# Optimization experiments

Measured on AMD Instinct MI355X. Metric: run time of the kernel, lower is better.

Reference implementation:

```python
import jax, jax.numpy as jnp
import numpy as np

N_NODES = 4096
IN_FEAT = 256
N_HEADS = 8
N_HIDDEN = 64  # out_features // n_heads
NEG_SLOPE = 0.2
EDGE_PROB = 0.05


def setup_inputs() -> dict:
    key = jax.random.key(0)
    k1, k2, k3, k4 = jax.random.split(key, 4)
    h = jax.random.normal(k1, (N_NODES, IN_FEAT), dtype=jnp.float32)
    # binary adjacency mask [N, N, 1] (broadcast over heads), as in the torch asserts
    adj_mat = (jax.random.uniform(k2, (N_NODES, N_NODES, 1)) < EDGE_PROB).astype(jnp.float32)
    # nn.Linear(in_features, n_heads*n_hidden, bias=False) weight: [H*F, in]
    W = jax.random.normal(k3, (N_HEADS * N_HIDDEN, IN_FEAT), dtype=jnp.float32) / np.sqrt(IN_FEAT)
    # nn.Linear(2*n_hidden, 1, bias=False) weight, flattened: [2*F]
    a = jax.random.normal(k4, (2 * N_HIDDEN,), dtype=jnp.float32) / np.sqrt(2 * N_HIDDEN)
    return {"h": h, "adj_mat": adj_mat, "W": W, "a": a}


def reference(h, adj_mat, W, a):
    n = h.shape[0]
    # g: [N, H, F]
    g = (h @ W.T).reshape(n, N_HEADS, N_HIDDEN)
    # attn(cat[g_i, g_j]) == a_l . g_i + a_r . g_j  (linear, no bias)
    a_l = a[:N_HIDDEN]
    a_r = a[N_HIDDEN:]
    el = jnp.einsum('ihf,f->ih', g, a_l)  # [N, H]
    er = jnp.einsum('jhf,f->jh', g, a_r)  # [N, H]
    e = jax.nn.leaky_relu(el[:, None, :] + er[None, :, :], NEG_SLOPE)  # [N, N, H]
    # note: original multiplies scores by adjacency (not masked_fill)
    e = e * adj_mat  # adj broadcasts over heads
    att = jax.nn.softmax(e, axis=1)  # softmax over source nodes j
    # dropout is identity at eval (dropout_rate=0.0)
    out = jnp.einsum('ijh,jhf->ihf', att, g)  # [N, H, F]
    return out.reshape(n, N_HEADS * N_HIDDEN)
```

## Files before the change

### kernel.cpp

```cpp
#include <hip/hip_runtime.h>

#define N_NODES 4096
#define IN_FEAT 256
#define N_HEADS 8
#define N_HIDDEN 64
#define OUT_FEAT (N_HEADS * N_HIDDEN)
#define NEG_SLOPE 0.2f

typedef _Float16 half8 __attribute__((ext_vector_type(8)));
typedef float floatx4 __attribute__((ext_vector_type(4)));

__global__ __launch_bounds__(256) void produce(
    const float* __restrict__ H, const float* __restrict__ adj,
    const float* __restrict__ Wt, const float* __restrict__ a,
    _Float16* __restrict__ GT16, float* __restrict__ elT,
    float* __restrict__ eR1, float* __restrict__ eR2,
    unsigned long long* __restrict__ bits) {
  __shared__ _Float16 SM[4 * 64 * 64];
  const int t = threadIdx.x;
  const int bx = blockIdx.x, by = blockIdx.y;

  if (by >= 8) {
    const int c = bx * 8 + (by - 8);
    const size_t W0 = (size_t)c * 512;
    const int wv = t >> 6, lane = t & 63;
    for (int k0 = 0; k0 < 128; k0 += 8) {
      float v[8];
#pragma unroll
      for (int k = 0; k < 8; ++k)
        v[k] = adj[(W0 + wv * 128 + k0 + k) * 64 + lane];
#pragma unroll
      for (int k = 0; k < 8; ++k) {
        unsigned long long m = __ballot(v[k] != 0.f);
        if (lane == 0) bits[W0 + wv * 128 + k0 + k] = m;
      }
    }
    return;
  }

  _Float16* Ah = SM;
  _Float16* Al = SM + 4096;
  _Float16* Bh = SM + 8192;
  _Float16* Bl = SM + 12288;
  const int w = t >> 6, l = t & 63;
  const int n16 = l & 15, q = l >> 4;
  const int bi = bx, bo = by;
  const int m0 = bi * 64 + w * 16;

  floatx4 acc[4];
#pragma unroll
  for (int ct = 0; ct < 4; ++ct) acc[ct] = (floatx4)0.f;

  for (int kc = 0; kc < 4; ++kc) {
    if (kc) __syncthreads();
#pragma unroll
    for (int p = 0; p < 4; ++p) {
      const int idx = p * 256 + t;
      const int r = idx >> 4;
      const int c4 = (idx & 15) << 2;
      const int dst = r * 64 + ((((idx & 15) >> 1)) ^ (r & 7)) * 8 + (idx & 1) * 4;
      float4 hv = *(const float4*)(H + (size_t)(bi * 64 + r) * IN_FEAT + kc * 64 + c4);
      float4 wv = *(const float4*)(Wt + (size_t)(bo * 64 + r) * IN_FEAT + kc * 64 + c4);
      union { _Float16 h[4]; int2 d; } hh_, hl_, wh_, wl_;
      hh_.h[0] = (_Float16)hv.x; hh_.h[1] = (_Float16)hv.y;
      hh_.h[2] = (_Float16)hv.z; hh_.h[3] = (_Float16)hv.w;
      hl_.h[0] = (_Float16)(hv.x - (float)hh_.h[0]);
      hl_.h[1] = (_Float16)(hv.y - (float)hh_.h[1]);
      hl_.h[2] = (_Float16)(hv.z - (float)hh_.h[2]);
      hl_.h[3] = (_Float16)(hv.w - (float)hh_.h[3]);
      wh_.h[0] = (_Float16)wv.x; wh_.h[1] = (_Float16)wv.y;
      wh_.h[2] = (_Float16)wv.z; wh_.h[3] = (_Float16)wv.w;
      wl_.h[0] = (_Float16)(wv.x - (float)wh_.h[0]);
      wl_.h[1] = (_Float16)(wv.y - (float)wh_.h[1]);
      wl_.h[2] = (_Float16)(wv.z - (float)wh_.h[2]);
      wl_.h[3] = (_Float16)(wv.w - (float)wh_.h[3]);
      *(int2*)&Ah[dst] = hh_.d;
      *(int2*)&Al[dst] = hl_.d;
      *(int2*)&Bh[dst] = wh_.d;
      *(int2*)&Bl[dst] = wl_.d;
    }
    __syncthreads();
#pragma unroll
    for (int ks = 0; ks < 2; ++ks) {
      const int ao = (w * 16 + n16) * 64 + (((ks << 2) + q) ^ (n16 & 7)) * 8;
      half8 Afh = *(const half8*)&Ah[ao];
      half8 Afl = *(const half8*)&Al[ao];
#pragma unroll
      for (int ct = 0; ct < 4; ++ct) {
        const int bofs = (ct * 16 + n16) * 64 + (((ks << 2) + q) ^ (n16 & 7)) * 8;
        half8 Bfh = *(const half8*)&Bh[bofs];
        half8 Bfl = *(const half8*)&Bl[bofs];
        acc[ct] = __builtin_amdgcn_mfma_f32_16x16x32_f16(Afh, Bfh, acc[ct], 0, 0, 0);
        acc[ct] = __builtin_amdgcn_mfma_f32_16x16x32_f16(Afl, Bfh, acc[ct], 0, 0, 0);
        acc[ct] = __builtin_amdgcn_mfma_f32_16x16x32_f16(Afh, Bfl, acc[ct], 0, 0, 0);
      }
    }
  }

  float aLv[4], aRv[4];
#pragma unroll
  for (int ct = 0; ct < 4; ++ct) {
    aLv[ct] = a[ct * 16 + n16];
    aRv[ct] = a[64 + ct * 16 + n16];
  }
#pragma unroll
  for (int reg = 0; reg < 4; ++reg) {
    float sl = 0.f, sr = 0.f;
#pragma unroll
    for (int ct = 0; ct < 4; ++ct) {
      sl = fmaf(acc[ct][reg], aLv[ct], sl);
      sr = fmaf(acc[ct][reg], aRv[ct], sr);
    }
#pragma unroll
    for (int off = 1; off < 16; off <<= 1) {
      sl += __shfl_xor(sl, off);
      sr += __shfl_xor(sr, off);
    }
    if (n16 == 0) {
      const int rowi = m0 + q * 4 + reg;
      elT[(size_t)bo * N_NODES + rowi] = sl;
      eR1[(size_t)bo * N_NODES + rowi] = __expf(sr);
      eR2[(size_t)bo * N_NODES + rowi] = __expf(0.2f * sr);
    }
  }

  __syncthreads();
  _Float16* LG = SM;
#pragma unroll
  for (int ct = 0; ct < 4; ++ct)
#pragma unroll
    for (int reg = 0; reg < 4; ++reg)
      LG[(w * 16 + q * 4 + reg) * 72 + ct * 16 + n16] = (_Float16)acc[ct][reg];
  __syncthreads();
  {
    const int f = t >> 2, jq = t & 3;
    union { _Float16 hh[16]; int4 v[2]; } u;
#pragma unroll
    for (int k = 0; k < 16; ++k) u.hh[k] = LG[(jq * 16 + k) * 72 + f];
    _Float16* dst = GT16 + (size_t)(bo * 64 + f) * N_NODES + bi * 64 + jq * 16;
    *(int4*)dst = u.v[0];
    *(int4*)(dst + 8) = u.v[1];
  }
}

__global__ __launch_bounds__(512) void attn_v5(
    const unsigned long long* __restrict__ bits, const _Float16* __restrict__ GT16,
    const float* __restrict__ elT, const float* __restrict__ eR1,
    const float* __restrict__ eR2, float* __restrict__ out) {
  __shared__ __align__(16) unsigned char GtRaw[2][2][8192];
  __shared__ float eRs1[2][2][64], eRs2[2][2][64];
  __shared__ unsigned long long bitsS[2][2][64];
  __shared__ float eL1s[64], eL2s[64];
  __shared__ float ZBuf[2][64];

  const int t = threadIdx.x;
  const int ib = blockIdx.x, h = blockIdx.y;
  const int i0 = ib * 64;
  const int w = t >> 6, l = t & 63, n16 = l & 15, q = l >> 4;
  const int jh = w >> 2, rt = w & 3;

  auto stage = [&](int par, int step) {
    const int sf = t >> 3, sseg = t & 7;
#pragma unroll
    for (int g = 0; g < 2; ++g) {
      const _Float16* src =
          GT16 + (size_t)(h * 64 + sf) * N_NODES + g * 2048 + step * 64 + sseg * 8;
      int4 v = *(const int4*)src;
      *(int4*)&((_Float16*)GtRaw[g][par])[sf * 64 + (sseg ^ (sf & 7)) * 8] = v;
    }
    if (t < 128) {
      eRs1[t >> 6][par][t & 63] =
          eR1[(size_t)h * N_NODES + (t >> 6) * 2048 + step * 64 + (t & 63)];
    } else if (t < 256) {
      const int u = t - 128;
      eRs2[u >> 6][par][u & 63] =
          eR2[(size_t)h * N_NODES + (u >> 6) * 2048 + step * 64 + (u & 63)];
    } else if (t < 384) {
      const int u = t - 256;
      bitsS[u >> 6][par][u & 63] =
          bits[(size_t)(i0 + (u & 63)) * 64 + (u >> 6) * 32 + step];
    }
  };

  if (t < 64) {
    float e = elT[(size_t)h * N_NODES + i0 + t];
    eL1s[t] = __expf(e);
    eL2s[t] = __expf(0.2f * e);
  }
  stage(0, 0);
  __syncthreads();

  const float eL1 = eL1s[rt * 16 + n16];
  const float eL2 = eL2s[rt * 16 + n16];
  half8 Bones;
#pragma unroll
  for (int k = 0; k < 8; ++k) Bones[k] = (n16 == 0) ? (_Float16)1.f : (_Float16)0.f;

  floatx4 acc[4];
#pragma unroll
  for (int ft = 0; ft < 4; ++ft) acc[ft] = (floatx4)0.f;
  floatx4 acc5 = (floatx4)0.f;

  int par = 0;
  for (int step = 0; step < 32; ++step) {
    if (step + 1 < 32) stage(par ^ 1, step + 1);
    const unsigned long long bv = bitsS[jh][par][rt * 16 + n16];
    const _Float16* gt = (const _Float16*)GtRaw[jh][par];
#pragma unroll
    for (int ks = 0; ks < 2; ++ks) {
      const int j8 = ks * 32 + q * 8;
      const unsigned byte = (unsigned)(bv >> j8) & 0xffu;
      float4 r1a = *(const float4*)&eRs1[jh][par][j8];
      float4 r1b = *(const float4*)&eRs1[jh][par][j8 + 4];
      float4 r2a = *(const float4*)&eRs2[jh][par][j8];
      float4 r2b = *(const float4*)&eRs2[jh][par][j8 + 4];
      float r1[8] = {r1a.x, r1a.y, r1a.z, r1a.w, r1b.x, r1b.y, r1b.z, r1b.w};
      float r2[8] = {r2a.x, r2a.y, r2a.z, r2a.w, r2b.x, r2b.y, r2b.z, r2b.w};
      half8 Af;
#pragma unroll
      for (int k = 0; k < 8; ++k) {
        const float pv = fmaxf(eL1 * r1[k], eL2 * r2[k]);
        const float p = ((byte >> k) & 1u) ? pv : 1.0f;
        Af[k] = (_Float16)p;
      }
#pragma unroll
      for (int ft = 0; ft < 4; ++ft) {
        half8 Bf = *(const half8*)&gt[(ft * 16 + n16) * 64 + (((ks << 2) + q) ^ (n16 & 7)) * 8];
        acc[ft] = __builtin_amdgcn_mfma_f32_16x16x32_f16(Af, Bf, acc[ft], 0, 0, 0);
      }
      acc5 = __builtin_amdgcn_mfma_f32_16x16x32_f16(Af, Bones, acc5, 0, 0, 0);
    }
    __syncthreads();
    par ^= 1;
  }

  float* comb1 = (float*)GtRaw;
  if (jh == 1) {
#pragma unroll
    for (int ft = 0; ft < 4; ++ft)
#pragma unroll
      for (int reg = 0; reg < 4; ++reg)
        comb1[(rt * 16 + q * 4 + reg) * 68 + ft * 16 + n16] = acc[ft][reg];
    if (n16 == 0) {
#pragma unroll
      for (int reg = 0; reg < 4; ++reg) ZBuf[0][rt * 16 + q * 4 + reg] = acc5[reg];
    }
  }
  __syncthreads();
  if (jh == 0) {
#pragma unroll
    for (int ft = 0; ft < 4; ++ft)
#pragma unroll
      for (int reg = 0; reg < 4; ++reg)
        acc[ft][reg] += comb1[(rt * 16 + q * 4 + reg) * 68 + ft * 16 + n16];
    if (n16 == 0) {
#pragma unroll
      for (int reg = 0; reg < 4; ++reg)
        ZBuf[1][rt * 16 + q * 4 + reg] = acc5[reg] + ZBuf[0][rt * 16 + q * 4 + reg];
    }
  }
  __syncthreads();
  if (jh == 0) {
#pragma unroll
    for (int reg = 0; reg < 4; ++reg) {
      const int row = rt * 16 + q * 4 + reg;
      const float invz = 1.f / ZBuf[1][row];
      float* op = out + (size_t)(i0 + row) * OUT_FEAT + h * 64;
#pragma unroll
      for (int ft = 0; ft < 4; ++ft) op[ft * 16 + n16] = acc[ft][reg] * invz;
    }
  }
}

extern "C" void kernel_launch(void* const* d_in, const int* in_sizes, int n_in,
                              void* d_out, int out_size, void* d_ws, size_t ws_size,
                              hipStream_t stream) {
  const float* h   = (const float*)d_in[0];
  const float* adj = (const float*)d_in[1];
  const float* W   = (const float*)d_in[2];
  const float* a   = (const float*)d_in[3];
  float* out = (float*)d_out;

  char* ws = (char*)d_ws;
  _Float16* GT16 = (_Float16*)ws;
  unsigned long long* bits = (unsigned long long*)(ws + 4u * 1024 * 1024);
  float* elT = (float*)(ws + 6u * 1024 * 1024);
  float* eR1 = (float*)(ws + 6u * 1024 * 1024 + 128 * 1024);
  float* eR2 = (float*)(ws + 6u * 1024 * 1024 + 256 * 1024);

  produce<<<dim3(64, 16), 256, 0, stream>>>(h, adj, W, a, GT16, elT, eR1, eR2, bits);
  attn_v5<<<dim3(64, 8), 512, 0, stream>>>(bits, GT16, elT, eR1, eR2, out);
}
```

Measured before the change: 169.2 us.

## Halve attention block rows, store exp factors in fp16, use packed half math

```diff
diff --git a/kernel.cpp b/kernel.cpp
--- a/kernel.cpp
+++ b/kernel.cpp
@@ -8,13 +8,14 @@
 #define NEG_SLOPE 0.2f
 
 typedef _Float16 half8 __attribute__((ext_vector_type(8)));
+typedef _Float16 h2 __attribute__((ext_vector_type(2)));
 typedef float floatx4 __attribute__((ext_vector_type(4)));
 
 __global__ __launch_bounds__(256) void produce(
     const float* __restrict__ H, const float* __restrict__ adj,
     const float* __restrict__ Wt, const float* __restrict__ a,
     _Float16* __restrict__ GT16, float* __restrict__ elT,
-    float* __restrict__ eR1, float* __restrict__ eR2,
+    _Float16* __restrict__ eR1h, _Float16* __restrict__ eR2h,
     unsigned long long* __restrict__ bits) {
   __shared__ _Float16 SM[4 * 64 * 64];
   const int t = threadIdx.x;
@@ -119,8 +120,8 @@
     if (n16 == 0) {
       const int rowi = m0 + q * 4 + reg;
       elT[(size_t)bo * N_NODES + rowi] = sl;
-      eR1[(size_t)bo * N_NODES + rowi] = __expf(sr);
-      eR2[(size_t)bo * N_NODES + rowi] = __expf(0.2f * sr);
+      eR1h[(size_t)bo * N_NODES + rowi] = (_Float16)__expf(sr);
+      eR2h[(size_t)bo * N_NODES + rowi] = (_Float16)__expf(0.2f * sr);
     }
   }
 
@@ -143,55 +144,53 @@
   }
 }
 
-__global__ __launch_bounds__(512) void attn_v5(
+__global__ __launch_bounds__(256) void attn_v6(
     const unsigned long long* __restrict__ bits, const _Float16* __restrict__ GT16,
-    const float* __restrict__ elT, const float* __restrict__ eR1,
-    const float* __restrict__ eR2, float* __restrict__ out) {
-  __shared__ __align__(16) unsigned char GtRaw[2][2][8192];
-  __shared__ float eRs1[2][2][64], eRs2[2][2][64];
-  __shared__ unsigned long long bitsS[2][2][64];
-  __shared__ float eL1s[64], eL2s[64];
-  __shared__ float ZBuf[2][64];
+    const float* __restrict__ elT, const _Float16* __restrict__ eR1h,
+    const _Float16* __restrict__ eR2h, float* __restrict__ out) {
+  __shared__ __align__(16) _Float16 Gt[2][2][4096];
+  __shared__ __align__(16) _Float16 eRs1[2][2][64];
+  __shared__ __align__(16) _Float16 eRs2[2][2][64];
+  __shared__ uint2 bitsS[2][2][32];
+  __shared__ float eL1s[32], eL2s[32];
+  __shared__ float Zh1[32], Zfull[32];
 
   const int t = threadIdx.x;
   const int ib = blockIdx.x, h = blockIdx.y;
-  const int i0 = ib * 64;
+  const int i0 = ib * 32;
   const int w = t >> 6, l = t & 63, n16 = l & 15, q = l >> 4;
-  const int jh = w >> 2, rt = w & 3;
-
-  auto stage = [&](int par, int step) {
-    const int sf = t >> 3, sseg = t & 7;
-#pragma unroll
-    for (int g = 0; g < 2; ++g) {
-      const _Float16* src =
-          GT16 + (size_t)(h * 64 + sf) * N_NODES + g * 2048 + step * 64 + sseg * 8;
-      int4 v = *(const int4*)src;
-      *(int4*)&((_Float16*)GtRaw[g][par])[sf * 64 + (sseg ^ (sf & 7)) * 8] = v;
-    }
-    if (t < 128) {
-      eRs1[t >> 6][par][t & 63] =
-          eR1[(size_t)h * N_NODES + (t >> 6) * 2048 + step * 64 + (t & 63)];
-    } else if (t < 256) {
-      const int u = t - 128;
-      eRs2[u >> 6][par][u & 63] =
-          eR2[(size_t)h * N_NODES + (u >> 6) * 2048 + step * 64 + (u & 63)];
-    } else if (t < 384) {
-      const int u = t - 256;
-      bitsS[u >> 6][par][u & 63] =
-          bits[(size_t)(i0 + (u & 63)) * 64 + (u >> 6) * 32 + step];
-    }
-  };
-
-  if (t < 64) {
+  const int rt = w & 1, jh = w >> 1;
+
+  const int gjh = t >> 7, sf = (t >> 1) & 63, hrow = t & 1;
+  const _Float16* gsrc = GT16 + (size_t)(h * 64 + sf) * N_NODES + gjh * 2048 + hrow * 32;
+  const int era = (t >> 3) & 1, erjh = t >> 4, erseg = t & 7;
+  const int bro = (t - 32) & 31, brjh = (t - 32) >> 5;
+
+  if (t < 32) {
     float e = elT[(size_t)h * N_NODES + i0 + t];
     eL1s[t] = __expf(e);
     eL2s[t] = __expf(0.2f * e);
   }
-  stage(0, 0);
-  __syncthreads();
-
-  const float eL1 = eL1s[rt * 16 + n16];
-  const float eL2 = eL2s[rt * 16 + n16];
+  {
+#pragma unroll
+    for (int g = 0; g < 4; ++g) {
+      int4 v = *(const int4*)(gsrc + g * 8);
+      *(int4*)&Gt[0][gjh][sf * 64 + ((hrow * 4 + g) ^ (sf & 7)) * 8] = v;
+    }
+    if (t < 32) {
+      const _Float16* esrc = (era ? eR2h : eR1h) + (size_t)h * N_NODES + erjh * 2048 + erseg * 8;
+      int4 v = *(const int4*)esrc;
+      *(int4*)&(era ? eRs2 : eRs1)[0][erjh][erseg * 8] = v;
+    } else if (t < 96) {
+      bitsS[0][brjh][bro] = *(const uint2*)&bits[(size_t)(i0 + bro) * 64 + brjh * 32];
+    }
+  }
+  __syncthreads();
+
+  const _Float16 e1f = (_Float16)eL1s[rt * 16 + n16];
+  const _Float16 e2f = (_Float16)eL2s[rt * 16 + n16];
+  const h2 eL1h2 = {e1f, e1f};
+  const h2 eL2h2 = {e2f, e2f};
   half8 Bones;
 #pragma unroll
   for (int k = 0; k < 8; ++k) Bones[k] = (n16 == 0) ? (_Float16)1.f : (_Float16)0.f;
@@ -203,26 +202,43 @@
 
   int par = 0;
   for (int step = 0; step < 32; ++step) {
-    if (step + 1 < 32) stage(par ^ 1, step + 1);
-    const unsigned long long bv = bitsS[jh][par][rt * 16 + n16];
-    const _Float16* gt = (const _Float16*)GtRaw[jh][par];
+    int4 gv[4]; int4 ev; uint2 bv2;
+    const bool more = (step + 1 < 32);
+    if (more) {
+      const _Float16* gs = gsrc + (size_t)(step + 1) * 64;
+#pragma unroll
+      for (int g = 0; g < 4; ++g) gv[g] = *(const int4*)(gs + g * 8);
+      if (t < 32) {
+        const _Float16* esrc = (era ? eR2h : eR1h) + (size_t)h * N_NODES + erjh * 2048 +
+                               (step + 1) * 64 + erseg * 8;
+        ev = *(const int4*)esrc;
+      } else if (t < 96) {
+        bv2 = *(const uint2*)&bits[(size_t)(i0 + bro) * 64 + brjh * 32 + step + 1];
+      }
+    }
+    const uint2 bw = bitsS[par][jh][rt * 16 + n16];
+    const _Float16* gt = &Gt[par][jh][0];
 #pragma unroll
     for (int ks = 0; ks < 2; ++ks) {
-      const int j8 = ks * 32 + q * 8;
-      const unsigned byte = (unsigned)(bv >> j8) & 0xffu;
-      float4 r1a = *(const float4*)&eRs1[jh][par][j8];
-      float4 r1b = *(const float4*)&eRs1[jh][par][j8 + 4];
-      float4 r2a = *(const float4*)&eRs2[jh][par][j8];
-      float4 r2b = *(const float4*)&eRs2[jh][par][j8 + 4];
-      float r1[8] = {r1a.x, r1a.y, r1a.z, r1a.w, r1b.x, r1b.y, r1b.z, r1b.w};
-      float r2[8] = {r2a.x, r2a.y, r2a.z, r2a.w, r2b.x, r2b.y, r2b.z, r2b.w};
-      half8 Af;
-#pragma unroll
-      for (int k = 0; k < 8; ++k) {
-        const float pv = fmaxf(eL1 * r1[k], eL2 * r2[k]);
-        const float p = ((byte >> k) & 1u) ? pv : 1.0f;
-        Af[k] = (_Float16)p;
-      }
+      const unsigned dw = ks ? bw.y : bw.x;
+      const unsigned byte = (dw >> (q * 8)) & 0xffu;
+      uint4 r1 = *(const uint4*)&eRs1[par][jh][ks * 32 + q * 8];
+      uint4 r2 = *(const uint4*)&eRs2[par][jh][ks * 32 + q * 8];
+      const unsigned r1a[4] = {r1.x, r1.y, r1.z, r1.w};
+      const unsigned r2a[4] = {r2.x, r2.y, r2.z, r2.w};
+      unsigned pr[4];
+#pragma unroll
+      for (int kk = 0; kk < 4; ++kk) {
+        h2 pa = eL1h2 * __builtin_bit_cast(h2, r1a[kk]);
+        h2 pb = eL2h2 * __builtin_bit_cast(h2, r2a[kk]);
+        h2 pv = __builtin_elementwise_max(pa, pb);
+        unsigned y = (byte >> (2 * kk)) & 3u;
+        unsigned b01 = (y | (y << 15)) & 0x00010001u;
+        unsigned keep = b01 * 0xffffu;
+        pr[kk] = (__builtin_bit_cast(unsigned, pv) & keep) | (0x3C003C00u & ~keep);
+      }
+      const uint4 prv = {pr[0], pr[1], pr[2], pr[3]};
+      half8 Af = __builtin_bit_cast(half8, prv);
 #pragma unroll
       for (int ft = 0; ft < 4; ++ft) {
         half8 Bf = *(const half8*)&gt[(ft * 16 + n16) * 64 + (((ks << 2) + q) ^ (n16 & 7)) * 8];
@@ -230,20 +246,31 @@
       }
       acc5 = __builtin_amdgcn_mfma_f32_16x16x32_f16(Af, Bones, acc5, 0, 0, 0);
     }
+    if (more) {
+      const int np = par ^ 1;
+#pragma unroll
+      for (int g = 0; g < 4; ++g)
+        *(int4*)&Gt[np][gjh][sf * 64 + ((hrow * 4 + g) ^ (sf & 7)) * 8] = gv[g];
+      if (t < 32) {
+        *(int4*)&(era ? eRs2 : eRs1)[np][erjh][erseg * 8] = ev;
+      } else if (t < 96) {
+        bitsS[np][brjh][bro] = bv2;
+      }
+    }
     __syncthreads();
     par ^= 1;
   }
 
-  float* comb1 = (float*)GtRaw;
+  float* comb = (float*)&Gt[0][0][0];
   if (jh == 1) {
 #pragma unroll
     for (int ft = 0; ft < 4; ++ft)
 #pragma unroll
       for (int reg = 0; reg < 4; ++reg)
-        comb1[(rt * 16 + q * 4 + reg) * 68 + ft * 16 + n16] = acc[ft][reg];
+        comb[(rt * 16 + q * 4 + reg) * 68 + ft * 16 + n16] = acc[ft][reg];
     if (n16 == 0) {
 #pragma unroll
-      for (int reg = 0; reg < 4; ++reg) ZBuf[0][rt * 16 + q * 4 + reg] = acc5[reg];
+      for (int reg = 0; reg < 4; ++reg) Zh1[rt * 16 + q * 4 + reg] = acc5[reg];
     }
   }
   __syncthreads();
@@ -252,11 +279,13 @@
     for (int ft = 0; ft < 4; ++ft)
 #pragma unroll
       for (int reg = 0; reg < 4; ++reg)
-        acc[ft][reg] += comb1[(rt * 16 + q * 4 + reg) * 68 + ft * 16 + n16];
+        acc[ft][reg] += comb[(rt * 16 + q * 4 + reg) * 68 + ft * 16 + n16];
     if (n16 == 0) {
 #pragma unroll
-      for (int reg = 0; reg < 4; ++reg)
-        ZBuf[1][rt * 16 + q * 4 + reg] = acc5[reg] + ZBuf[0][rt * 16 + q * 4 + reg];
+      for (int reg = 0; reg < 4; ++reg) {
+        const int row = rt * 16 + q * 4 + reg;
+        Zfull[row] = acc5[reg] + Zh1[row];
+      }
     }
   }
   __syncthreads();
@@ -264,7 +293,7 @@
 #pragma unroll
     for (int reg = 0; reg < 4; ++reg) {
       const int row = rt * 16 + q * 4 + reg;
-      const float invz = 1.f / ZBuf[1][row];
+      const float invz = 1.f / Zfull[row];
       float* op = out + (size_t)(i0 + row) * OUT_FEAT + h * 64;
 #pragma unroll
       for (int ft = 0; ft < 4; ++ft) op[ft * 16 + n16] = acc[ft][reg] * invz;
@@ -285,9 +314,9 @@
   _Float16* GT16 = (_Float16*)ws;
   unsigned long long* bits = (unsigned long long*)(ws + 4u * 1024 * 1024);
   float* elT = (float*)(ws + 6u * 1024 * 1024);
-  float* eR1 = (float*)(ws + 6u * 1024 * 1024 + 128 * 1024);
-  float* eR2 = (float*)(ws + 6u * 1024 * 1024 + 256 * 1024);
-
-  produce<<<dim3(64, 16), 256, 0, stream>>>(h, adj, W, a, GT16, elT, eR1, eR2, bits);
-  attn_v5<<<dim3(64, 8), 512, 0, stream>>>(bits, GT16, elT, eR1, eR2, out);
+  _Float16* eR1h = (_Float16*)(ws + 6u * 1024 * 1024 + 128 * 1024);
+  _Float16* eR2h = (_Float16*)(ws + 6u * 1024 * 1024 + 192 * 1024);
+
+  produce<<<dim3(64, 16), 256, 0, stream>>>(h, adj, W, a, GT16, elT, eR1h, eR2h, bits);
+  attn_v6<<<dim3(128, 8), 256, 0, stream>>>(bits, GT16, elT, eR1h, eR2h, out);
 }
```

Result: faster. 160.6 us (-5.1%).
